# Kernel tuning notes

Hardware: AMD Instinct MI355X
Metric: run time of the kernel (lower is better)

## Reference

```python
import jax, jax.numpy as jnp
import numpy as np
import math

NUM_HEADS = 8


def setup_inputs() -> dict:
    key = jax.random.key(0)
    ks = jax.random.split(key, 6)
    b, s, e = 4, 2048, 512
    x = jax.random.normal(ks[0], (b, s, e), dtype=jnp.float32)
    # 0/1 adjacency matrix as float (it multiplies the scores in the module)
    adj = jax.random.randint(ks[1], (b, s, s), 0, 2).astype(jnp.float32)
    scale = 0.02
    Wqkv_w = jax.random.normal(ks[2], (3 * e, e), dtype=jnp.float32) * scale
    Wqkv_b = jax.random.normal(ks[3], (3 * e,), dtype=jnp.float32) * scale
    out_w = jax.random.normal(ks[4], (e, e), dtype=jnp.float32) * scale
    out_b = jax.random.normal(ks[5], (e,), dtype=jnp.float32) * scale
    return {"x": x, "adj": adj, "Wqkv_w": Wqkv_w, "Wqkv_b": Wqkv_b,
            "out_w": out_w, "out_b": out_b}


def reference(x, adj, Wqkv_w, Wqkv_b, out_w, out_b):
    b, s, e = x.shape
    h = NUM_HEADS
    d = e // h
    # fused qkv projection: (b, s, 3*e) -> (b, s, 3, h, d)
    qkv = (x @ Wqkv_w.T + Wqkv_b).reshape(b, s, 3, h, d)
    qkv = jnp.transpose(qkv, (2, 0, 3, 1, 4))  # (3, b, h, s, d)
    q, k, v = qkv[0], qkv[1], qkv[2]
    inv_sqrt_d = 1.0 / math.sqrt(d)
    scores = jnp.einsum('bhqd,bhkd->bhqk', q, k) * inv_sqrt_d
    scores = jnp.clip(scores * adj[:, None, :, :], -10000.0, 10000.0)
    attn = jax.nn.softmax(scores, axis=-1)
    out = jnp.einsum('bhqk,bhkd->bhqd', attn, v)
    out = jnp.transpose(out, (0, 2, 1, 3)).reshape(b, s, e)  # (b, s, h*d)
    return out @ out_w.T + out_b
```

## Files before the change

### kernel.cpp

```cpp
#include <hip/hip_runtime.h>


typedef __attribute__((ext_vector_type(8))) short bf16x8;
typedef __attribute__((ext_vector_type(4))) float f32x4;
typedef __attribute__((ext_vector_type(4))) unsigned short ushort4v;
typedef __attribute__((ext_vector_type(4))) _Float16 f16x4;

#if __has_builtin(__builtin_amdgcn_exp2f)
#define EXP2F(x) __builtin_amdgcn_exp2f(x)
#else
#define EXP2F(x) exp2f(x)
#endif

#define QSCALE 0.18033688011112042f

__device__ __forceinline__ unsigned short f2bf(float f) {
  unsigned int u = __float_as_uint(f);
  u += 0x7FFFu + ((u >> 16) & 1u);
  return (unsigned short)(u >> 16);
}
__device__ __forceinline__ unsigned short f2h(float f) {
  union { _Float16 h; unsigned short u; } cv;
  cv.h = (_Float16)f;
  return cv.u;
}

__global__ __launch_bounds__(256) void prep_k(const float* __restrict__ x,
                                              unsigned short* __restrict__ x_bf,
                                              const float* __restrict__ wqkv,
                                              unsigned short* __restrict__ wqkv_bf,
                                              const float* __restrict__ outw,
                                              unsigned short* __restrict__ outw_bf,
                                              const float* __restrict__ adj,
                                              unsigned long long* __restrict__ abits) {
  const int bid = blockIdx.x;
  if (bid < 5120) {
    const float* in; unsigned short* out; int i;
    if (bid < 4096) { in = x; out = x_bf; i = bid * 256 + threadIdx.x; }
    else if (bid < 4864) { in = wqkv; out = wqkv_bf; i = (bid - 4096) * 256 + threadIdx.x; }
    else { in = outw; out = outw_bf; i = (bid - 4864) * 256 + threadIdx.x; }
    float4 v = ((const float4*)in)[i];
    ushort4v o;
    o[0] = f2bf(v.x); o[1] = f2bf(v.y); o[2] = f2bf(v.z); o[3] = f2bf(v.w);
    ((ushort4v*)out)[i] = o;
  } else {
    const int gw = (bid - 5120) * 4 + (threadIdx.x >> 6);
    const int l = threadIdx.x & 63;
    const int b = gw >> 11, q = gw & 2047;
    const float* row = adj + ((size_t)b * 2048 + q) * 2048;
    unsigned long long* ob = abits + (size_t)b * 65536 + q;
#pragma unroll 4
    for (int kt = 0; kt < 32; ++kt) {
      const float v = row[kt * 64 + l];
      const unsigned long long m = __ballot(v != 0.f);
      if (l == 0) ob[(size_t)kt * 2048] = m;
    }
  }
}

template <int MODE>
__global__ __launch_bounds__(256, 3) void gemm128_k(const unsigned short* __restrict__ A,
                                                    const unsigned short* __restrict__ Bt,
                                                    const float* __restrict__ bias, int Kdim,
                                                    int Ntiles, unsigned short* __restrict__ q_out,
                                                    unsigned short* __restrict__ k_out,
                                                    unsigned short* __restrict__ v_out,
                                                    float* __restrict__ f_out) {
  __shared__ union {
    struct { unsigned short A[2][128][40], B[2][128][40]; } s;
    unsigned short T[64][136];
  } u;

  const int t = threadIdx.x;
  const int lane = t & 63, w = t >> 6, ln = lane & 15, quad = lane >> 4;
  const int mt = blockIdx.x / Ntiles, nt = blockIdx.x % Ntiles;
  const int wm = (w >> 1) * 64, wn = (w & 1) * 64;
  const int strow = t >> 2, stcol = (t & 3) * 8;

  const size_t abase = (size_t)(mt * 128 + strow) * Kdim + stcol;
  const size_t bbase = (size_t)(nt * 128 + strow) * Kdim + stcol;

  f32x4 acc[4][4];
#pragma unroll
  for (int i = 0; i < 4; ++i)
#pragma unroll
    for (int j = 0; j < 4; ++j) acc[i][j] = (f32x4){0.f, 0.f, 0.f, 0.f};

  bf16x8 a0 = *(const bf16x8*)(A + abase);
  bf16x8 a1 = *(const bf16x8*)(A + abase + (size_t)64 * Kdim);
  bf16x8 b0 = *(const bf16x8*)(Bt + bbase);
  bf16x8 b1 = *(const bf16x8*)(Bt + bbase + (size_t)64 * Kdim);
  *(bf16x8*)&u.s.A[0][strow][stcol] = a0;
  *(bf16x8*)&u.s.A[0][64 + strow][stcol] = a1;
  *(bf16x8*)&u.s.B[0][strow][stcol] = b0;
  *(bf16x8*)&u.s.B[0][64 + strow][stcol] = b1;
  __syncthreads();

  const int iters = Kdim >> 5;
  for (int it = 0; it < iters; ++it) {
    const int cur = it & 1, nxt = cur ^ 1;

    const int kn = ((it + 1) << 5) & (Kdim - 1);
    a0 = *(const bf16x8*)(A + abase + kn);
    a1 = *(const bf16x8*)(A + abase + (size_t)64 * Kdim + kn);
    b0 = *(const bf16x8*)(Bt + bbase + kn);
    b1 = *(const bf16x8*)(Bt + bbase + (size_t)64 * Kdim + kn);

    bf16x8 bfr[4];
#pragma unroll
    for (int nf = 0; nf < 4; ++nf)
      bfr[nf] = *(const bf16x8*)&u.s.B[cur][wn + nf * 16 + ln][quad * 8];
#pragma unroll
    for (int mf = 0; mf < 4; ++mf) {
      bf16x8 af = *(const bf16x8*)&u.s.A[cur][wm + mf * 16 + ln][quad * 8];
#pragma unroll
      for (int nf = 0; nf < 4; ++nf)
        acc[mf][nf] = __builtin_amdgcn_mfma_f32_16x16x32_bf16(af, bfr[nf], acc[mf][nf], 0, 0, 0);
    }

    if (it + 1 < iters) {
      *(bf16x8*)&u.s.A[nxt][strow][stcol] = a0;
      *(bf16x8*)&u.s.A[nxt][64 + strow][stcol] = a1;
      *(bf16x8*)&u.s.B[nxt][strow][stcol] = b0;
      *(bf16x8*)&u.s.B[nxt][64 + strow][stcol] = b1;
      __syncthreads();
    }
  }

  if (MODE == 0 && nt >= 8) {
    const int bb = mt >> 4, sq0 = (mt & 15) * 128;
#pragma unroll
    for (int half = 0; half < 2; ++half) {
      __syncthreads();
      if ((w & 1) == half) {
#pragma unroll
        for (int nf = 0; nf < 4; ++nf) {
          const float bv = bias[nt * 128 + half * 64 + nf * 16 + ln];
#pragma unroll
          for (int mf = 0; mf < 4; ++mf)
#pragma unroll
            for (int r = 0; r < 4; ++r)
              u.T[nf * 16 + ln][wm + mf * 16 + quad * 4 + r] = f2h(acc[mf][nf][r] + bv);
        }
      }
      __syncthreads();
#pragma unroll
      for (int rep = 0; rep < 4; ++rep) {
        const int row = rep * 16 + (t >> 4), c = t & 15;
        const bf16x8 val = *(const bf16x8*)&u.T[row][c * 8];
        const int hd = (nt - 8) * 128 + half * 64 + row;
        const int hh = hd >> 6, dd = hd & 63;
        *(bf16x8*)(v_out + ((size_t)(bb * 8 + hh) * 64 + dd) * 2048 + sq0 + c * 8) = val;
      }
    }
    return;
  }

#pragma unroll
  for (int mf = 0; mf < 4; ++mf) {
    const int m = mt * 128 + wm + mf * 16 + quad * 4;
#pragma unroll
    for (int nf = 0; nf < 4; ++nf) {
      const int n = nt * 128 + wn + nf * 16 + ln;
      const float bv = bias[n];
      if (MODE == 0) {
        const int hd = n & 511;
        const int hh = hd >> 6, dd = hd & 63;
        const int bb = m >> 11, sq = m & 2047;
        if (n < 512) {
#pragma unroll
          for (int r = 0; r < 4; ++r)
            q_out[((size_t)(bb * 8 + hh) * 2048 + sq + r) * 64 + dd] =
                f2bf((acc[mf][nf][r] + bv) * QSCALE);
        } else {
#pragma unroll
          for (int r = 0; r < 4; ++r)
            k_out[((size_t)(bb * 8 + hh) * 2048 + sq + r) * 64 + dd] = f2bf(acc[mf][nf][r] + bv);
        }
      } else {
#pragma unroll
        for (int r = 0; r < 4; ++r) f_out[(size_t)(m + r) * 512 + n] = acc[mf][nf][r] + bv;
      }
    }
  }
}

__global__ __launch_bounds__(256, 2) void attn_k(const unsigned short* __restrict__ Qg,
                                                 const unsigned short* __restrict__ Kg,
                                                 const unsigned short* __restrict__ Vg,
                                                 const unsigned long long* __restrict__ Mg,
                                                 unsigned short* __restrict__ Og) {
  __shared__ unsigned short K_lds[2][64][72];
  __shared__ unsigned short V_lds[2][64][72];
  __shared__ unsigned long long M_lds[2][128];

  const int t = threadIdx.x;
  const int w = t >> 6, lane = t & 63, ln = lane & 15, quad = lane >> 4;
  const int bh = blockIdx.x & 31, qt = blockIdx.x >> 5, bb = bh >> 3;
  const int sbase = qt * 128;

  const unsigned short* Qp = Qg + (size_t)bh * (2048 * 64);
  const unsigned short* Kp = Kg + (size_t)bh * (2048 * 64);
  const unsigned short* Vp = Vg + (size_t)bh * (64 * 2048);
  const unsigned long long* Mp = Mg + (size_t)bb * 65536 + sbase;

  bf16x8 qf[2][2];
#pragma unroll
  for (int qg = 0; qg < 2; ++qg) {
    const int qrow = sbase + w * 32 + qg * 16 + ln;
    qf[qg][0] = *(const bf16x8*)(Qp + (size_t)qrow * 64 + quad * 8);
    qf[qg][1] = *(const bf16x8*)(Qp + (size_t)qrow * 64 + 32 + quad * 8);
  }

  const _Float16 one_h = (_Float16)((ln == 0) ? 1.0f : 0.0f);
  const f16x4 vf_one = (f16x4){one_h, one_h, one_h, one_h};

  f32x4 acc_o[2][4];
#pragma unroll
  for (int qg = 0; qg < 2; ++qg)
#pragma unroll
    for (int dg = 0; dg < 4; ++dg) acc_o[qg][dg] = (f32x4){0.f, 0.f, 0.f, 0.f};
  f32x4 acc_1[2] = {(f32x4){0.f, 0.f, 0.f, 0.f}, (f32x4){0.f, 0.f, 0.f, 0.f}};

  const int strow = t >> 2;
  const int stcol = (t & 3) * 16;

  bf16x8 kr0 = *(const bf16x8*)(Kp + (size_t)strow * 64 + stcol);
  bf16x8 kr1 = *(const bf16x8*)(Kp + (size_t)strow * 64 + stcol + 8);
  bf16x8 vr0 = *(const bf16x8*)(Vp + (size_t)strow * 2048 + stcol);
  bf16x8 vr1 = *(const bf16x8*)(Vp + (size_t)strow * 2048 + stcol + 8);
  unsigned long long mreg = (w < 2) ? Mp[w * 64 + lane] : 0ull;
  *(bf16x8*)&K_lds[0][strow][stcol] = kr0;
  *(bf16x8*)&K_lds[0][strow][stcol + 8] = kr1;
  *(bf16x8*)&V_lds[0][strow][stcol] = vr0;
  *(bf16x8*)&V_lds[0][strow][stcol + 8] = vr1;
  if (w < 2) M_lds[0][w * 64 + lane] = mreg;
  __syncthreads();

  for (int kt = 0; kt < 32; ++kt) {
    const int cur = kt & 1, nxt = cur ^ 1;

    const int k0n = ((kt + 1) & 31) * 64;
    kr0 = *(const bf16x8*)(Kp + (size_t)(k0n + strow) * 64 + stcol);
    kr1 = *(const bf16x8*)(Kp + (size_t)(k0n + strow) * 64 + stcol + 8);
    vr0 = *(const bf16x8*)(Vp + (size_t)strow * 2048 + k0n + stcol);
    vr1 = *(const bf16x8*)(Vp + (size_t)strow * 2048 + k0n + stcol + 8);
    if (w < 2) mreg = Mp[((kt + 1) & 31) * 2048 + w * 64 + lane];

    f32x4 sc[2][4];
#pragma unroll
    for (int nf = 0; nf < 4; ++nf) {
      bf16x8 kf0 = *(const bf16x8*)&K_lds[cur][nf * 16 + ln][quad * 8];
      bf16x8 kf1 = *(const bf16x8*)&K_lds[cur][nf * 16 + ln][32 + quad * 8];
#pragma unroll
      for (int qg = 0; qg < 2; ++qg) {
        f32x4 z = (f32x4){0.f, 0.f, 0.f, 0.f};
        z = __builtin_amdgcn_mfma_f32_16x16x32_bf16(kf0, qf[qg][0], z, 0, 0, 0);
        sc[qg][nf] = __builtin_amdgcn_mfma_f32_16x16x32_bf16(kf1, qf[qg][1], z, 0, 0, 0);
      }
    }

    f16x4 vfa[4][4];
#pragma unroll
    for (int ks = 0; ks < 4; ++ks)
#pragma unroll
      for (int dg = 0; dg < 4; ++dg)
        vfa[ks][dg] = *(const f16x4*)&V_lds[cur][dg * 16 + ln][ks * 16 + quad * 4];

    f16x4 pa[2][4];
#pragma unroll
    for (int qg = 0; qg < 2; ++qg) {
      const unsigned long long m64 = M_lds[cur][w * 32 + qg * 16 + ln];
#pragma unroll
      for (int nf = 0; nf < 4; ++nf) {
        const unsigned nib = (unsigned)(m64 >> (nf * 16 + quad * 4)) & 0xFu;
#pragma unroll
        for (int r = 0; r < 4; ++r) {
          const float s = (nib >> r) & 1u ? sc[qg][nf][r] : 0.f;
          pa[qg][nf][r] = (_Float16)EXP2F(s);
        }
      }
    }

#pragma unroll
    for (int ks = 0; ks < 4; ++ks)
#pragma unroll
      for (int qg = 0; qg < 2; ++qg) {
#pragma unroll
        for (int dg = 0; dg < 4; ++dg)
          acc_o[qg][dg] =
              __builtin_amdgcn_mfma_f32_16x16x16f16(pa[qg][ks], vfa[ks][dg], acc_o[qg][dg], 0, 0, 0);
        acc_1[qg] = __builtin_amdgcn_mfma_f32_16x16x16f16(pa[qg][ks], vf_one, acc_1[qg], 0, 0, 0);
      }

    if (kt < 31) {
      *(bf16x8*)&K_lds[nxt][strow][stcol] = kr0;
      *(bf16x8*)&K_lds[nxt][strow][stcol + 8] = kr1;
      *(bf16x8*)&V_lds[nxt][strow][stcol] = vr0;
      *(bf16x8*)&V_lds[nxt][strow][stcol + 8] = vr1;
      if (w < 2) M_lds[nxt][w * 64 + lane] = mreg;
      __syncthreads();
    }
  }

  unsigned short* Op = Og + (size_t)bb * 2048 * 512 + (size_t)(bh & 7) * 64;
#pragma unroll
  for (int qg = 0; qg < 2; ++qg)
#pragma unroll
    for (int r = 0; r < 4; ++r) {
      const float inv = 1.0f / __shfl(acc_1[qg][r], quad * 16);
      const int sq = sbase + w * 32 + qg * 16 + quad * 4 + r;
#pragma unroll
      for (int dg = 0; dg < 4; ++dg)
        Op[(size_t)sq * 512 + dg * 16 + ln] = f2bf(acc_o[qg][dg][r] * inv);
    }
}

extern "C" void kernel_launch(void* const* d_in, const int* in_sizes, int n_in, void* d_out,
                              int out_size, void* d_ws, size_t ws_size, hipStream_t stream) {
  const float* x = (const float*)d_in[0];
  const float* adj = (const float*)d_in[1];
  const float* wqkv = (const float*)d_in[2];
  const float* bqkv = (const float*)d_in[3];
  const float* outw = (const float*)d_in[4];
  const float* outb = (const float*)d_in[5];
  float* out = (float*)d_out;

  char* ws = (char*)d_ws;
  unsigned short* x_bf = (unsigned short*)(ws);
  unsigned short* wqkv_bf = (unsigned short*)(ws + 8388608);
  unsigned short* outw_bf = (unsigned short*)(ws + 9961472);
  unsigned long long* abits = (unsigned long long*)(ws + 10485760);
  unsigned short* Qb = (unsigned short*)(ws + 27262976);
  unsigned short* Kb = (unsigned short*)(ws + 35651584);
  unsigned short* Vb = (unsigned short*)(ws + 44040192);
  unsigned short* Ob = (unsigned short*)(ws + 52428800);

  prep_k<<<7168, 256, 0, stream>>>(x, x_bf, wqkv, wqkv_bf, outw, outw_bf, adj, abits);

  gemm128_k<0><<<768, 256, 0, stream>>>(x_bf, wqkv_bf, bqkv, 512, 12, Qb, Kb, Vb, nullptr);

  attn_k<<<512, 256, 0, stream>>>(Qb, Kb, Vb, abits, Ob);

  gemm128_k<1><<<256, 256, 0, stream>>>(Ob, outw_bf, outb, 512, 4, nullptr, nullptr, nullptr, out);
}
```

Baseline: 225.8 us.

## Split attention over key halves with atomic fp32 accumulation, normalize in output GEMM

The attention kernel now splits the key range into two halves, doubling the grid to 1024 blocks, and raises launch bounds to 4 waves per SIMD. Each half atomically adds unnormalized partial outputs and row sums into fp32 buffers, zeroed by a memset that reuses the x_bf region. The output projection GEMM loads these fp32 partials, divides by the row sum and converts to bf16 on the fly. The aim is better occupancy and load balance in attention. The cost is an extra memset, fp32 atomic traffic, and a heavier A-load path in the final GEMM.

```diff
diff --git a/kernel.cpp b/kernel.cpp
--- a/kernel.cpp
+++ b/kernel.cpp
@@ -65,7 +65,9 @@
                                                     int Ntiles, unsigned short* __restrict__ q_out,
                                                     unsigned short* __restrict__ k_out,
                                                     unsigned short* __restrict__ v_out,
-                                                    float* __restrict__ f_out) {
+                                                    float* __restrict__ f_out,
+                                                    const float* __restrict__ Of,
+                                                    const float* __restrict__ Lf) {
   __shared__ union {
     struct { unsigned short A[2][128][40], B[2][128][40]; } s;
     unsigned short T[64][136];
@@ -80,14 +82,34 @@
   const size_t abase = (size_t)(mt * 128 + strow) * Kdim + stcol;
   const size_t bbase = (size_t)(nt * 128 + strow) * Kdim + stcol;
 
+  auto ldA1 = [&](int mrow, int c) -> bf16x8 {
+    const float4 p0 = *(const float4*)(Of + (size_t)mrow * 512 + c);
+    const float4 p1 = *(const float4*)(Of + (size_t)mrow * 512 + c + 4);
+    const int bb = mrow >> 11, sq = mrow & 2047, hh = c >> 6;
+    const float li = 1.0f / Lf[((bb << 3) + hh) * 2048 + sq];
+    bf16x8 r;
+    r[0] = (short)f2bf(p0.x * li); r[1] = (short)f2bf(p0.y * li);
+    r[2] = (short)f2bf(p0.z * li); r[3] = (short)f2bf(p0.w * li);
+    r[4] = (short)f2bf(p1.x * li); r[5] = (short)f2bf(p1.y * li);
+    r[6] = (short)f2bf(p1.z * li); r[7] = (short)f2bf(p1.w * li);
+    return r;
+  };
+  const int mrow0 = mt * 128 + strow, mrow1 = mt * 128 + 64 + strow;
+
   f32x4 acc[4][4];
 #pragma unroll
   for (int i = 0; i < 4; ++i)
 #pragma unroll
     for (int j = 0; j < 4; ++j) acc[i][j] = (f32x4){0.f, 0.f, 0.f, 0.f};
 
-  bf16x8 a0 = *(const bf16x8*)(A + abase);
-  bf16x8 a1 = *(const bf16x8*)(A + abase + (size_t)64 * Kdim);
+  bf16x8 a0, a1;
+  if (MODE == 0) {
+    a0 = *(const bf16x8*)(A + abase);
+    a1 = *(const bf16x8*)(A + abase + (size_t)64 * Kdim);
+  } else {
+    a0 = ldA1(mrow0, stcol);
+    a1 = ldA1(mrow1, stcol);
+  }
   bf16x8 b0 = *(const bf16x8*)(Bt + bbase);
   bf16x8 b1 = *(const bf16x8*)(Bt + bbase + (size_t)64 * Kdim);
   *(bf16x8*)&u.s.A[0][strow][stcol] = a0;
@@ -101,8 +123,13 @@
     const int cur = it & 1, nxt = cur ^ 1;
 
     const int kn = ((it + 1) << 5) & (Kdim - 1);
-    a0 = *(const bf16x8*)(A + abase + kn);
-    a1 = *(const bf16x8*)(A + abase + (size_t)64 * Kdim + kn);
+    if (MODE == 0) {
+      a0 = *(const bf16x8*)(A + abase + kn);
+      a1 = *(const bf16x8*)(A + abase + (size_t)64 * Kdim + kn);
+    } else {
+      a0 = ldA1(mrow0, stcol + kn);
+      a1 = ldA1(mrow1, stcol + kn);
+    }
     b0 = *(const bf16x8*)(Bt + bbase + kn);
     b1 = *(const bf16x8*)(Bt + bbase + (size_t)64 * Kdim + kn);
 
@@ -185,19 +212,22 @@
   }
 }
 
-__global__ __launch_bounds__(256, 2) void attn_k(const unsigned short* __restrict__ Qg,
+__global__ __launch_bounds__(256, 4) void attn_k(const unsigned short* __restrict__ Qg,
                                                  const unsigned short* __restrict__ Kg,
                                                  const unsigned short* __restrict__ Vg,
                                                  const unsigned long long* __restrict__ Mg,
-                                                 unsigned short* __restrict__ Og) {
+                                                 float* __restrict__ Of,
+                                                 float* __restrict__ Lf) {
   __shared__ unsigned short K_lds[2][64][72];
   __shared__ unsigned short V_lds[2][64][72];
   __shared__ unsigned long long M_lds[2][128];
 
   const int t = threadIdx.x;
   const int w = t >> 6, lane = t & 63, ln = lane & 15, quad = lane >> 4;
-  const int bh = blockIdx.x & 31, qt = blockIdx.x >> 5, bb = bh >> 3;
+  const int bh = blockIdx.x & 31, qt = (blockIdx.x >> 5) & 15, half = blockIdx.x >> 9;
+  const int bb = bh >> 3;
   const int sbase = qt * 128;
+  const int kt0 = half * 16;
 
   const unsigned short* Qp = Qg + (size_t)bh * (2048 * 64);
   const unsigned short* Kp = Kg + (size_t)bh * (2048 * 64);
@@ -225,27 +255,31 @@
   const int strow = t >> 2;
   const int stcol = (t & 3) * 16;
 
-  bf16x8 kr0 = *(const bf16x8*)(Kp + (size_t)strow * 64 + stcol);
-  bf16x8 kr1 = *(const bf16x8*)(Kp + (size_t)strow * 64 + stcol + 8);
-  bf16x8 vr0 = *(const bf16x8*)(Vp + (size_t)strow * 2048 + stcol);
-  bf16x8 vr1 = *(const bf16x8*)(Vp + (size_t)strow * 2048 + stcol + 8);
-  unsigned long long mreg = (w < 2) ? Mp[w * 64 + lane] : 0ull;
-  *(bf16x8*)&K_lds[0][strow][stcol] = kr0;
-  *(bf16x8*)&K_lds[0][strow][stcol + 8] = kr1;
-  *(bf16x8*)&V_lds[0][strow][stcol] = vr0;
-  *(bf16x8*)&V_lds[0][strow][stcol + 8] = vr1;
-  if (w < 2) M_lds[0][w * 64 + lane] = mreg;
+  {
+    const int k0 = kt0 * 64;
+    bf16x8 kr0 = *(const bf16x8*)(Kp + (size_t)(k0 + strow) * 64 + stcol);
+    bf16x8 kr1 = *(const bf16x8*)(Kp + (size_t)(k0 + strow) * 64 + stcol + 8);
+    bf16x8 vr0 = *(const bf16x8*)(Vp + (size_t)strow * 2048 + k0 + stcol);
+    bf16x8 vr1 = *(const bf16x8*)(Vp + (size_t)strow * 2048 + k0 + stcol + 8);
+    unsigned long long mreg = (w < 2) ? Mp[(size_t)kt0 * 2048 + w * 64 + lane] : 0ull;
+    *(bf16x8*)&K_lds[0][strow][stcol] = kr0;
+    *(bf16x8*)&K_lds[0][strow][stcol + 8] = kr1;
+    *(bf16x8*)&V_lds[0][strow][stcol] = vr0;
+    *(bf16x8*)&V_lds[0][strow][stcol + 8] = vr1;
+    if (w < 2) M_lds[0][w * 64 + lane] = mreg;
+  }
   __syncthreads();
 
-  for (int kt = 0; kt < 32; ++kt) {
-    const int cur = kt & 1, nxt = cur ^ 1;
-
-    const int k0n = ((kt + 1) & 31) * 64;
-    kr0 = *(const bf16x8*)(Kp + (size_t)(k0n + strow) * 64 + stcol);
-    kr1 = *(const bf16x8*)(Kp + (size_t)(k0n + strow) * 64 + stcol + 8);
-    vr0 = *(const bf16x8*)(Vp + (size_t)strow * 2048 + k0n + stcol);
-    vr1 = *(const bf16x8*)(Vp + (size_t)strow * 2048 + k0n + stcol + 8);
-    if (w < 2) mreg = Mp[((kt + 1) & 31) * 2048 + w * 64 + lane];
+  for (int ktl = 0; ktl < 16; ++ktl) {
+    const int cur = ktl & 1, nxt = cur ^ 1;
+
+    const int ktn = kt0 + ((ktl + 1) & 15);
+    const int k0n = ktn * 64;
+    bf16x8 kr0 = *(const bf16x8*)(Kp + (size_t)(k0n + strow) * 64 + stcol);
+    bf16x8 kr1 = *(const bf16x8*)(Kp + (size_t)(k0n + strow) * 64 + stcol + 8);
+    bf16x8 vr0 = *(const bf16x8*)(Vp + (size_t)strow * 2048 + k0n + stcol);
+    bf16x8 vr1 = *(const bf16x8*)(Vp + (size_t)strow * 2048 + k0n + stcol + 8);
+    unsigned long long mreg = (w < 2) ? Mp[(size_t)ktn * 2048 + w * 64 + lane] : 0ull;
 
     f32x4 sc[2][4];
 #pragma unroll
@@ -293,7 +327,7 @@
         acc_1[qg] = __builtin_amdgcn_mfma_f32_16x16x16f16(pa[qg][ks], vf_one, acc_1[qg], 0, 0, 0);
       }
 
-    if (kt < 31) {
+    if (ktl < 15) {
       *(bf16x8*)&K_lds[nxt][strow][stcol] = kr0;
       *(bf16x8*)&K_lds[nxt][strow][stcol + 8] = kr1;
       *(bf16x8*)&V_lds[nxt][strow][stcol] = vr0;
@@ -303,17 +337,24 @@
     }
   }
 
-  unsigned short* Op = Og + (size_t)bb * 2048 * 512 + (size_t)(bh & 7) * 64;
+  float* Ofp = Of + (size_t)bb * 2048 * 512 + (size_t)(bh & 7) * 64;
 #pragma unroll
   for (int qg = 0; qg < 2; ++qg)
 #pragma unroll
     for (int r = 0; r < 4; ++r) {
-      const float inv = 1.0f / __shfl(acc_1[qg][r], quad * 16);
       const int sq = sbase + w * 32 + qg * 16 + quad * 4 + r;
 #pragma unroll
       for (int dg = 0; dg < 4; ++dg)
-        Op[(size_t)sq * 512 + dg * 16 + ln] = f2bf(acc_o[qg][dg][r] * inv);
-    }
+        atomicAdd(&Ofp[(size_t)sq * 512 + dg * 16 + ln], acc_o[qg][dg][r]);
+    }
+  if (ln == 0) {
+    float* Lfp = Lf + bh * 2048;
+#pragma unroll
+    for (int qg = 0; qg < 2; ++qg)
+#pragma unroll
+      for (int r = 0; r < 4; ++r)
+        atomicAdd(&Lfp[sbase + w * 32 + qg * 16 + quad * 4 + r], acc_1[qg][r]);
+  }
 }
 
 extern "C" void kernel_launch(void* const* d_in, const int* in_sizes, int n_in, void* d_out,
@@ -329,18 +370,23 @@
   char* ws = (char*)d_ws;
   unsigned short* x_bf = (unsigned short*)(ws);
   unsigned short* wqkv_bf = (unsigned short*)(ws + 8388608);
-  unsigned short* outw_bf = (unsigned short*)(ws + 9961472);
-  unsigned long long* abits = (unsigned long long*)(ws + 10485760);
-  unsigned short* Qb = (unsigned short*)(ws + 27262976);
-  unsigned short* Kb = (unsigned short*)(ws + 35651584);
-  unsigned short* Vb = (unsigned short*)(ws + 44040192);
-  unsigned short* Ob = (unsigned short*)(ws + 52428800);
+  float* Of = (float*)(ws);
+  float* Lf = (float*)(ws + 16777216);
+  unsigned short* outw_bf = (unsigned short*)(ws + 17301504);
+  unsigned long long* abits = (unsigned long long*)(ws + 17825792);
+  unsigned short* Qb = (unsigned short*)(ws + 19922944);
+  unsigned short* Kb = (unsigned short*)(ws + 28311552);
+  unsigned short* Vb = (unsigned short*)(ws + 36700160);
 
   prep_k<<<7168, 256, 0, stream>>>(x, x_bf, wqkv, wqkv_bf, outw, outw_bf, adj, abits);
 
-  gemm128_k<0><<<768, 256, 0, stream>>>(x_bf, wqkv_bf, bqkv, 512, 12, Qb, Kb, Vb, nullptr);
-
-  attn_k<<<512, 256, 0, stream>>>(Qb, Kb, Vb, abits, Ob);
-
-  gemm128_k<1><<<256, 256, 0, stream>>>(Ob, outw_bf, outb, 512, 4, nullptr, nullptr, nullptr, out);
-}
+  gemm128_k<0><<<768, 256, 0, stream>>>(x_bf, wqkv_bf, bqkv, 512, 12, Qb, Kb, Vb, nullptr,
+                                        nullptr, nullptr);
+
+  hipMemsetAsync(Of, 0, 16777216 + 524288, stream);
+
+  attn_k<<<1024, 256, 0, stream>>>(Qb, Kb, Vb, abits, Of, Lf);
+
+  gemm128_k<1><<<256, 256, 0, stream>>>(nullptr, outw_bf, outb, 512, 4, nullptr, nullptr, nullptr,
+                                        out, Of, Lf);
+}
```

New measurement: 252.7 us. +11.9%, slower.
